# Kernel tuning notes

Hardware: AMD Instinct MI355X
Metric: run time of the kernel (lower is better)

Reference implementation:

```python
import jax, jax.numpy as jnp
import numpy as np

D_MODEL = 1024
D_INNER = 2048   # expand * d_model
D_STATE = 16
D_CONV = 4
DT_RANK = 64     # ceil(d_model / 16)
BATCH = 2
SEQLEN = 4096


def setup_inputs() -> dict:
    key = jax.random.key(0)
    ks = jax.random.split(key, 9)
    g = lambda k, shape, scale: jax.random.normal(k, shape, dtype=jnp.float32) * scale
    hidden_states = g(ks[0], (BATCH, SEQLEN, D_MODEL), 1.0)
    W_in = g(ks[1], (2 * D_INNER, D_MODEL), D_MODEL ** -0.5)
    conv_w = g(ks[2], (D_INNER, D_CONV), D_CONV ** -0.5)
    conv_b = g(ks[3], (D_INNER,), 0.02)
    x_proj_w = g(ks[4], (DT_RANK + 2 * D_STATE, D_INNER), D_INNER ** -0.5)
    dt_w = g(ks[5], (D_INNER, DT_RANK), DT_RANK ** -0.5)
    # dt bias init as in Mamba: inverse softplus of dt ~ U[log(1e-3), log(1e-1)]
    dt = jnp.exp(jax.random.uniform(ks[6], (D_INNER,), dtype=jnp.float32)
                 * (np.log(0.1) - np.log(0.001)) + np.log(0.001))
    dt = jnp.clip(dt, 1e-4, None)
    dt_b = dt + jnp.log(-jnp.expm1(-dt))
    # A_log init: log of [1..d_state] repeated per channel
    A_log = jnp.log(jnp.tile(jnp.arange(1, D_STATE + 1, dtype=jnp.float32), (D_INNER, 1)))
    D = jnp.ones((D_INNER,), dtype=jnp.float32)
    W_out = g(ks[7], (D_MODEL, D_INNER), D_INNER ** -0.5)
    return dict(hidden_states=hidden_states, W_in=W_in, conv_w=conv_w, conv_b=conv_b,
                x_proj_w=x_proj_w, dt_w=dt_w, dt_b=dt_b, A_log=A_log, D=D, W_out=W_out)


def reference(hidden_states, W_in, conv_w, conv_b, x_proj_w, dt_w, dt_b, A_log, D, W_out):
    B, L, _ = hidden_states.shape
    # in_proj + transpose -> (B, 2*Din, L)
    xz = jnp.einsum('bld,ed->bel', hidden_states, W_in)
    # nanotron (tp=1) splits via view(B, d_inner, 2, L): interleaved channels
    xz = xz.reshape(B, D_INNER, 2, L)
    x, z = xz[:, :, 0, :], xz[:, :, 1, :]          # (B, Din, L)
    # causal depthwise conv1d (pad left d_conv-1) + SiLU
    xc = jax.lax.conv_general_dilated(
        x, conv_w[:, None, :], window_strides=(1,), padding=[(D_CONV - 1, 0)],
        dimension_numbers=('NCH', 'OIH', 'NCH'), feature_group_count=D_INNER)
    x = jax.nn.silu(xc + conv_b[None, :, None])     # (B, Din, L)
    # x_proj -> dt, B, C
    x_dbl = jnp.einsum('bdl,ed->ble', x, x_proj_w)  # (B, L, dt_rank+2N)
    dt, Bm, Cm = jnp.split(x_dbl, [DT_RANK, DT_RANK + D_STATE], axis=-1)
    delta = jnp.einsum('blr,dr->bdl', dt, dt_w)     # (B, Din, L)
    delta = jax.nn.softplus(delta + dt_b[None, :, None])
    A = -jnp.exp(A_log)                             # (Din, N)
    # selective scan over time
    xs = (jnp.transpose(delta, (2, 0, 1)),          # (L, B, Din)
          jnp.transpose(x, (2, 0, 1)),              # (L, B, Din)
          jnp.transpose(Bm, (1, 0, 2)),             # (L, B, N)
          jnp.transpose(Cm, (1, 0, 2)))             # (L, B, N)

    def step(s, inp):
        d_t, x_t, B_t, C_t = inp
        s = s * jnp.exp(d_t[:, :, None] * A[None]) + (d_t * x_t)[:, :, None] * B_t[:, None, :]
        y_t = jnp.einsum('bdn,bn->bd', s, C_t)
        return s, y_t

    s0 = jnp.zeros((B, D_INNER, D_STATE), dtype=hidden_states.dtype)
    _, ys = jax.lax.scan(step, s0, xs)              # ys: (L, B, Din)
    y = jnp.transpose(ys, (1, 2, 0))                # (B, Din, L)
    y = y + D[None, :, None] * x
    y = y * jax.nn.silu(z)
    out = jnp.einsum('bdl,md->blm', y, W_out)       # (B, L, d_model)
    return out
```

## Files before the change

kernel.cpp:

```cpp
#include <hip/hip_runtime.h>
#include <hip/hip_bf16.h>

#define D_MODEL 1024
#define D_INNER 2048
#define D_STATE 16
#define DT_RANK 64
#define BATCH 2
#define SEQLEN 4096
#define BL (BATCH * SEQLEN)
#define NPROJ (DT_RANK + 2 * D_STATE)
#define CH 64
#define NCH (SEQLEN / CH)

typedef __attribute__((ext_vector_type(8))) short bf16x8;
typedef __attribute__((ext_vector_type(4))) float f32x4;
struct S4 { short x, y, z, w; };

__device__ __forceinline__ float sigmoidf_(float v) {
    return 1.0f / (1.0f + __expf(-v));
}

__device__ __forceinline__ unsigned short bf16_rne(float f) {
    unsigned u = __float_as_uint(f);
    unsigned r = u + 0x7FFFu + ((u >> 16) & 1u);
    return (unsigned short)(r >> 16);
}

__device__ __forceinline__ float bf2f(short s) {
    return __uint_as_float(((unsigned)(unsigned short)s) << 16);
}

__global__ __launch_bounds__(256)
void cvt_split(const float* __restrict__ in, short* __restrict__ hi,
               short* __restrict__ lo, int n4) {
    const int i = blockIdx.x * 256 + threadIdx.x;
    if (i >= n4) return;
    const float4 v = reinterpret_cast<const float4*>(in)[i];
    const float f[4] = {v.x, v.y, v.z, v.w};
    S4 h, l;
    short hb[4], lb[4];
#pragma unroll
    for (int j = 0; j < 4; ++j) {
        const unsigned short hh = bf16_rne(f[j]);
        const float hf = __uint_as_float((unsigned)hh << 16);
        hb[j] = (short)hh;
        lb[j] = (short)bf16_rne(f[j] - hf);
    }
    h.x = hb[0]; h.y = hb[1]; h.z = hb[2]; h.w = hb[3];
    l.x = lb[0]; l.y = lb[1]; l.z = lb[2]; l.w = lb[3];
    *reinterpret_cast<S4*>(hi + (size_t)i * 4) = h;
    *reinterpret_cast<S4*>(lo + (size_t)i * 4) = l;
}

__global__ __launch_bounds__(256)
void gemm_bf16x3(const short* __restrict__ Ahi, const short* __restrict__ Alo,
                 const short* __restrict__ Bhi, const short* __restrict__ Blo,
                 float* __restrict__ C, int K, int lda, int ldb, int ldc) {
    __shared__ short sA[2][128][32];
    __shared__ short sB[2][128][32];
    const int t = threadIdx.x;
    const int w = t >> 6, l = t & 63;

    const int nwg = gridDim.x * gridDim.y;
    int bid = blockIdx.y * gridDim.x + blockIdx.x;
    if ((nwg & 7) == 0) bid = (bid & 7) * (nwg >> 3) + (bid >> 3);
    const int m0 = (bid / gridDim.x) * 128, n0 = (bid % gridDim.x) * 128;
    const int wr = w >> 1, wc = w & 1;

    const short* gsrc;
    short* sdst;
    int ld, tile0;
    if (w == 0)      { gsrc = Ahi; sdst = &sA[0][0][0]; tile0 = m0; ld = lda; }
    else if (w == 1) { gsrc = Alo; sdst = &sA[1][0][0]; tile0 = m0; ld = lda; }
    else if (w == 2) { gsrc = Bhi; sdst = &sB[0][0][0]; tile0 = n0; ld = ldb; }
    else             { gsrc = Blo; sdst = &sB[1][0][0]; tile0 = n0; ld = ldb; }
    const size_t grow = (size_t)(tile0 + (l >> 2)) * ld + ((l & 3) << 3);

    f32x4 acc[4][4] = {};
    const int frow = l & 15;
    const int kb = (l >> 4) << 3;

    for (int k0 = 0; k0 < K; k0 += 32) {
        __syncthreads();
#pragma unroll
        for (int i = 0; i < 8; ++i) {
            const short* g = gsrc + grow + (size_t)(i << 4) * ld + k0;
            __builtin_amdgcn_global_load_lds(
                (const __attribute__((address_space(1))) void*)g,
                (__attribute__((address_space(3))) void*)(sdst + (i << 9)),
                16, 0, 0);
        }
        __syncthreads();

        bf16x8 a[2][4], b[2][4];
#pragma unroll
        for (int f = 0; f < 4; ++f) {
            a[0][f] = *reinterpret_cast<const bf16x8*>(&sA[0][wr * 64 + f * 16 + frow][kb]);
            a[1][f] = *reinterpret_cast<const bf16x8*>(&sA[1][wr * 64 + f * 16 + frow][kb]);
            b[0][f] = *reinterpret_cast<const bf16x8*>(&sB[0][wc * 64 + f * 16 + frow][kb]);
            b[1][f] = *reinterpret_cast<const bf16x8*>(&sB[1][wc * 64 + f * 16 + frow][kb]);
        }
#pragma unroll
        for (int fi = 0; fi < 4; ++fi)
#pragma unroll
            for (int fj = 0; fj < 4; ++fj) {
                acc[fi][fj] = __builtin_amdgcn_mfma_f32_16x16x32_bf16(
                    a[0][fi], b[0][fj], acc[fi][fj], 0, 0, 0);
                acc[fi][fj] = __builtin_amdgcn_mfma_f32_16x16x32_bf16(
                    a[1][fi], b[0][fj], acc[fi][fj], 0, 0, 0);
                acc[fi][fj] = __builtin_amdgcn_mfma_f32_16x16x32_bf16(
                    a[0][fi], b[1][fj], acc[fi][fj], 0, 0, 0);
            }
    }

    const int crow = (l >> 4) << 2;
    const int ccol = l & 15;
#pragma unroll
    for (int fi = 0; fi < 4; ++fi)
#pragma unroll
        for (int fj = 0; fj < 4; ++fj)
#pragma unroll
            for (int r = 0; r < 4; ++r)
                C[(size_t)(m0 + wr * 64 + fi * 16 + crow + r) * ldc
                  + (n0 + wc * 64 + fj * 16 + ccol)] = acc[fi][fj][r];
}

__global__ __launch_bounds__(256)
void gemm96(const short* __restrict__ Xhi, const short* __restrict__ Xlo,
            const short* __restrict__ Whi, const short* __restrict__ Wlo,
            float* __restrict__ C) {
    const int t = threadIdx.x;
    const int w = t >> 6, l = t & 63;
    const int m0 = blockIdx.x * 32;
    const int rfrag = (w >> 1) * 16;
    const int cbase = (w & 1) * 48;
    const int lrow = l & 15;
    const int koff0 = (l >> 4) << 3;
    f32x4 acc[3] = {};
    const size_t arow = (size_t)(m0 + rfrag + lrow) * D_INNER;
#pragma unroll 2
    for (int k0 = 0; k0 < D_INNER; k0 += 32) {
        const int ko = k0 + koff0;
        const bf16x8 ah = *reinterpret_cast<const bf16x8*>(Xhi + arow + ko);
        const bf16x8 al = *reinterpret_cast<const bf16x8*>(Xlo + arow + ko);
#pragma unroll
        for (int jj = 0; jj < 3; ++jj) {
            const size_t brow = (size_t)(cbase + jj * 16 + lrow) * D_INNER + ko;
            const bf16x8 bh = *reinterpret_cast<const bf16x8*>(Whi + brow);
            const bf16x8 bl = *reinterpret_cast<const bf16x8*>(Wlo + brow);
            acc[jj] = __builtin_amdgcn_mfma_f32_16x16x32_bf16(ah, bh, acc[jj], 0, 0, 0);
            acc[jj] = __builtin_amdgcn_mfma_f32_16x16x32_bf16(al, bh, acc[jj], 0, 0, 0);
            acc[jj] = __builtin_amdgcn_mfma_f32_16x16x32_bf16(ah, bl, acc[jj], 0, 0, 0);
        }
    }
    const int crow = (l >> 4) << 2;
#pragma unroll
    for (int jj = 0; jj < 3; ++jj)
#pragma unroll
        for (int r = 0; r < 4; ++r)
            C[(size_t)(m0 + rfrag + crow + r) * NPROJ + cbase + jj * 16 + lrow] = acc[jj][r];
}

template <int EPI>
__global__ __launch_bounds__(256)
void gemm_nt(const float* __restrict__ A, const float* __restrict__ B,
             float* __restrict__ C, int M, int N, int K,
             int lda, int ldb, int ldc, const float* __restrict__ bias) {
    constexpr int BM = 64, BN = 64, BK = 16, PAD = 4;
    __shared__ float As[BK][BM + PAD];
    __shared__ float Bs[BK][BN + PAD];
    const int t = threadIdx.x;
    const int tx = t & 15, ty = t >> 4;
    const int m0 = blockIdx.y * BM, n0 = blockIdx.x * BN;
    const int lrow = t >> 2;
    const int lcol = (t & 3) * 4;

    float acc[4][4] = {{0.f}};

    for (int k0 = 0; k0 < K; k0 += BK) {
        float4 av = *reinterpret_cast<const float4*>(
            A + (size_t)(m0 + lrow) * lda + k0 + lcol);
        float4 bv = *reinterpret_cast<const float4*>(
            B + (size_t)(n0 + lrow) * ldb + k0 + lcol);
        __syncthreads();
        As[lcol + 0][lrow] = av.x; As[lcol + 1][lrow] = av.y;
        As[lcol + 2][lrow] = av.z; As[lcol + 3][lrow] = av.w;
        Bs[lcol + 0][lrow] = bv.x; Bs[lcol + 1][lrow] = bv.y;
        Bs[lcol + 2][lrow] = bv.z; Bs[lcol + 3][lrow] = bv.w;
        __syncthreads();
#pragma unroll
        for (int k = 0; k < BK; ++k) {
            float4 a = *reinterpret_cast<const float4*>(&As[k][ty * 4]);
            float4 b = *reinterpret_cast<const float4*>(&Bs[k][tx * 4]);
            float ar[4] = {a.x, a.y, a.z, a.w};
            float br[4] = {b.x, b.y, b.z, b.w};
#pragma unroll
            for (int i = 0; i < 4; ++i)
#pragma unroll
                for (int j = 0; j < 4; ++j)
                    acc[i][j] = fmaf(ar[i], br[j], acc[i][j]);
        }
    }

#pragma unroll
    for (int i = 0; i < 4; ++i) {
        const int m = m0 + ty * 4 + i;
#pragma unroll
        for (int j = 0; j < 4; ++j) {
            const int n = n0 + tx * 4 + j;
            float v = acc[i][j];
            if (EPI == 1) {
                v += bias[n];
                v = fmaxf(v, 0.f) + log1pf(__expf(-fabsf(v)));
            }
            C[(size_t)m * ldc + n] = v;
        }
    }
}

__global__ __launch_bounds__(256)
void conv_silu_k(const float* __restrict__ xr, const float* __restrict__ cw,
                 const float* __restrict__ cb, short* __restrict__ xchi,
                 short* __restrict__ xclo) {
    const int idx = blockIdx.x * 256 + threadIdx.x;
    const int d = idx & (D_INNER - 1);
    const int bl = idx >> 11;
    const int l = bl & (SEQLEN - 1);
    const float4 w4 = *reinterpret_cast<const float4*>(cw + (size_t)d * 4);
    const float wj[4] = {w4.x, w4.y, w4.z, w4.w};
    float acc = cb[d];
#pragma unroll
    for (int j = 0; j < 4; ++j) {
        const int ll = l - 3 + j;
        if (ll >= 0)
            acc += xr[(size_t)(bl - 3 + j) * D_INNER + d] * wj[j];
    }
    const float v = acc * sigmoidf_(acc);
    const unsigned short hh = bf16_rne(v);
    xchi[idx] = (short)hh;
    xclo[idx] = (short)bf16_rne(v - __uint_as_float((unsigned)hh << 16));
}

__global__ __launch_bounds__(256)
void scan1(const float* __restrict__ delta, const short* __restrict__ xchi,
           const short* __restrict__ xclo, const float* __restrict__ dtbc,
           const float* __restrict__ A_log, float* __restrict__ sum_delta,
           float* __restrict__ S_end) {
    const int d = blockIdx.x * 256 + threadIdx.x;
    const int b = blockIdx.y;
    const int c = blockIdx.z;
    __shared__ float bc[CH][32];
    for (int i = threadIdx.x; i < CH * 32; i += 256) {
        const int row = i >> 5, col = i & 31;
        bc[row][col] = dtbc[(size_t)(b * SEQLEN + c * CH + row) * NPROJ + DT_RANK + col];
    }
    __syncthreads();
    float A[16];
#pragma unroll
    for (int n = 0; n < 16; ++n) A[n] = -__expf(A_log[(size_t)d * 16 + n]);
    float s[16] = {0.f};
    float sd = 0.f;
    const size_t base = ((size_t)b * SEQLEN + (size_t)c * CH) * D_INNER + d;
    for (int li = 0; li < CH; ++li) {
        const size_t o = base + (size_t)li * D_INNER;
        const float dl = delta[o];
        const float xv = bf2f(xchi[o]) + bf2f(xclo[o]);
        sd += dl;
        const float dx = dl * xv;
#pragma unroll
        for (int n = 0; n < 16; ++n) {
            const float a = __expf(dl * A[n]);
            s[n] = fmaf(s[n], a, dx * bc[li][n]);
        }
    }
    sum_delta[((size_t)c * BATCH + b) * D_INNER + d] = sd;
#pragma unroll
    for (int n = 0; n < 16; ++n)
        S_end[(((size_t)c * BATCH + b) * 16 + n) * D_INNER + d] = s[n];
}

__global__ __launch_bounds__(256)
void scan2(const float* __restrict__ sum_delta, float* __restrict__ S,
           const float* __restrict__ A_log) {
    const int idx = blockIdx.x * 256 + threadIdx.x;
    const int d = idx & (D_INNER - 1);
    const int n = (idx >> 11) & 15;
    const int b = idx >> 15;
    const float A = -__expf(A_log[(size_t)d * 16 + n]);
    float carry = 0.f;
    for (int c = 0; c < NCH; ++c) {
        const float sd = sum_delta[((size_t)c * BATCH + b) * D_INNER + d];
        const size_t o = (((size_t)c * BATCH + b) * 16 + n) * D_INNER + d;
        const float se = S[o];
        S[o] = carry;
        carry = fmaf(carry, __expf(sd * A), se);
    }
}

__global__ __launch_bounds__(256)
void scan3(float* __restrict__ delta ,
           const short* __restrict__ xchi, const short* __restrict__ xclo,
           const float* __restrict__ z, const float* __restrict__ dtbc,
           const float* __restrict__ A_log, const float* __restrict__ S_init,
           const float* __restrict__ Dp) {
    const int d = blockIdx.x * 256 + threadIdx.x;
    const int b = blockIdx.y;
    const int c = blockIdx.z;
    __shared__ float bc[CH][32];
    for (int i = threadIdx.x; i < CH * 32; i += 256) {
        const int row = i >> 5, col = i & 31;
        bc[row][col] = dtbc[(size_t)(b * SEQLEN + c * CH + row) * NPROJ + DT_RANK + col];
    }
    __syncthreads();
    float A[16];
#pragma unroll
    for (int n = 0; n < 16; ++n) A[n] = -__expf(A_log[(size_t)d * 16 + n]);
    float s[16];
#pragma unroll
    for (int n = 0; n < 16; ++n)
        s[n] = S_init[(((size_t)c * BATCH + b) * 16 + n) * D_INNER + d];
    const float Dv = Dp[d];
    const size_t base = ((size_t)b * SEQLEN + (size_t)c * CH) * D_INNER + d;
    for (int li = 0; li < CH; ++li) {
        const size_t o = base + (size_t)li * D_INNER;
        const float dl = delta[o];
        const float xv = bf2f(xchi[o]) + bf2f(xclo[o]);
        const float dx = dl * xv;
        float y = 0.f;
#pragma unroll
        for (int n = 0; n < 16; ++n) {
            const float a = __expf(dl * A[n]);
            s[n] = fmaf(s[n], a, dx * bc[li][n]);
            y = fmaf(s[n], bc[li][16 + n], y);
        }
        const float zv = z[o];
        delta[o] = (y + Dv * xv) * (zv * sigmoidf_(zv));
    }
}

extern "C" void kernel_launch(void* const* d_in, const int* in_sizes, int n_in,
                              void* d_out, int out_size, void* d_ws, size_t ws_size,
                              hipStream_t stream) {
    const float* hidden   = (const float*)d_in[0];
    const float* W_in     = (const float*)d_in[1];
    const float* conv_w   = (const float*)d_in[2];
    const float* conv_b   = (const float*)d_in[3];
    const float* x_proj_w = (const float*)d_in[4];
    const float* dt_w     = (const float*)d_in[5];
    const float* dt_b     = (const float*)d_in[6];
    const float* A_log    = (const float*)d_in[7];
    const float* Dp       = (const float*)d_in[8];
    const float* W_out    = (const float*)d_in[9];
    float* out = (float*)d_out;

    float* ws    = (float*)d_ws;
    float* xbuf  = ws;
    float* zbuf  = xbuf + (size_t)BL * D_INNER;
    float* xcreg = zbuf + (size_t)BL * D_INNER;
    float* dtbc  = xcreg + (size_t)BL * D_INNER;
    float* sumd  = dtbc + (size_t)BL * NPROJ;
    float* Send  = sumd + (size_t)NCH * BATCH * D_INNER;
    float* xpw   = Send + (size_t)NCH * BATCH * 16 * D_INNER;

    short* hxhi  = (short*)xcreg;
    short* hxlo  = hxhi + (size_t)BL * D_MODEL;
    short* winhi = hxlo + (size_t)BL * D_MODEL;
    short* winlo = winhi + (size_t)2 * D_INNER * D_MODEL;
    short* xpwhi = (short*)xpw;
    short* xpwlo = xpwhi + (size_t)NPROJ * D_INNER;

    const dim3 thr(256);

    cvt_split<<<dim3(BL * D_MODEL / 1024), thr, 0, stream>>>(hidden, hxhi, hxlo, BL * D_MODEL / 4);
    cvt_split<<<dim3(2 * D_INNER * D_MODEL / 1024), thr, 0, stream>>>(W_in, winhi, winlo, 2 * D_INNER * D_MODEL / 4);
    cvt_split<<<dim3(NPROJ * D_INNER / 1024), thr, 0, stream>>>(x_proj_w, xpwhi, xpwlo, NPROJ * D_INNER / 4);

    gemm_bf16x3<<<dim3(D_INNER / 128, BL / 128), thr, 0, stream>>>(
        hxhi, hxlo, winhi, winlo, xbuf, D_MODEL, D_MODEL, 2 * D_MODEL, D_INNER);
    gemm_bf16x3<<<dim3(D_INNER / 128, BL / 128), thr, 0, stream>>>(
        hxhi, hxlo, winhi + D_MODEL, winlo + D_MODEL, zbuf, D_MODEL, D_MODEL, 2 * D_MODEL, D_INNER);

    short* xchi = (short*)xcreg;
    short* xclo = xchi + (size_t)BL * D_INNER;
    conv_silu_k<<<dim3(BL * D_INNER / 256), thr, 0, stream>>>(xbuf, conv_w, conv_b, xchi, xclo);

    gemm96<<<dim3(BL / 32), thr, 0, stream>>>(xchi, xclo, xpwhi, xpwlo, dtbc);

    gemm_nt<1><<<dim3(D_INNER / 64, BL / 64), thr, 0, stream>>>(
        dtbc, dt_w, xbuf, BL, D_INNER, DT_RANK, NPROJ, DT_RANK, D_INNER, dt_b);

    scan1<<<dim3(D_INNER / 256, BATCH, NCH), thr, 0, stream>>>(
        xbuf, xchi, xclo, dtbc, A_log, sumd, Send);
    scan2<<<dim3(BATCH * 16 * D_INNER / 256), thr, 0, stream>>>(sumd, Send, A_log);
    scan3<<<dim3(D_INNER / 256, BATCH, NCH), thr, 0, stream>>>(
        xbuf, xchi, xclo, zbuf, dtbc, A_log, Send, Dp);

    short* yhi  = (short*)zbuf;
    short* ylo  = yhi + (size_t)BL * D_INNER;
    short* wohi = (short*)xcreg;
    short* wolo = wohi + (size_t)D_MODEL * D_INNER;
    cvt_split<<<dim3(BL * D_INNER / 1024), thr, 0, stream>>>(xbuf, yhi, ylo, BL * D_INNER / 4);
    cvt_split<<<dim3(D_MODEL * D_INNER / 1024), thr, 0, stream>>>(W_out, wohi, wolo, D_MODEL * D_INNER / 4);

    gemm_bf16x3<<<dim3(D_MODEL / 128, BL / 128), thr, 0, stream>>>(
        yhi, ylo, wohi, wolo, out, D_INNER, D_INNER, D_INNER, D_MODEL);
}
```

Baseline: 790.2 us.

## Swizzle GEMM LDS, move delta GEMM to MFMA, fuse y bf16 split into scan

Adds an XOR swizzle to the global-to-LDS load layout and the fragment reads of the bf16x3 GEMM to cut LDS bank conflicts. The fp32 SIMT delta GEMM (K=64) is replaced by the split-bf16 MFMA GEMM with a fused bias+softplus epilogue, and gemm96 now writes the dt columns as hi/lo bf16 directly. scan3 writes y already split into hi/lo bf16 into the xc buffers, which removes the separate cvt_split pass over y before the output projection. The trade-off is extra workspace for the dt and dt_w splits and reuse of buffers that must stay in the right order.

Result: faster. 762.9 us (-3.5%).

```diff
diff --git a/kernel.cpp b/kernel.cpp
--- a/kernel.cpp
+++ b/kernel.cpp
@@ -52,10 +52,12 @@
     *reinterpret_cast<S4*>(lo + (size_t)i * 4) = l;
 }
 
+template <int EPI>
 __global__ __launch_bounds__(256)
 void gemm_bf16x3(const short* __restrict__ Ahi, const short* __restrict__ Alo,
                  const short* __restrict__ Bhi, const short* __restrict__ Blo,
-                 float* __restrict__ C, int K, int lda, int ldb, int ldc) {
+                 float* __restrict__ C, int K, int lda, int ldb, int ldc,
+                 const float* __restrict__ bias) {
     __shared__ short sA[2][128][32];
     __shared__ short sB[2][128][32];
     const int t = threadIdx.x;
@@ -74,11 +76,12 @@
     else if (w == 1) { gsrc = Alo; sdst = &sA[1][0][0]; tile0 = m0; ld = lda; }
     else if (w == 2) { gsrc = Bhi; sdst = &sB[0][0][0]; tile0 = n0; ld = ldb; }
     else             { gsrc = Blo; sdst = &sB[1][0][0]; tile0 = n0; ld = ldb; }
-    const size_t grow = (size_t)(tile0 + (l >> 2)) * ld + ((l & 3) << 3);
+    const int kc_src = ((l & 3) ^ ((l >> 3) & 3)) << 3;
+    const size_t grow = (size_t)(tile0 + (l >> 2)) * ld + kc_src;
 
     f32x4 acc[4][4] = {};
     const int frow = l & 15;
-    const int kb = (l >> 4) << 3;
+    const int kb = (((l >> 4) ^ ((frow >> 1) & 3)) << 3);
 
     for (int k0 = 0; k0 < K; k0 += 32) {
         __syncthreads();
@@ -118,17 +121,25 @@
 #pragma unroll
     for (int fi = 0; fi < 4; ++fi)
 #pragma unroll
-        for (int fj = 0; fj < 4; ++fj)
-#pragma unroll
-            for (int r = 0; r < 4; ++r)
-                C[(size_t)(m0 + wr * 64 + fi * 16 + crow + r) * ldc
-                  + (n0 + wc * 64 + fj * 16 + ccol)] = acc[fi][fj][r];
+        for (int fj = 0; fj < 4; ++fj) {
+            const int n = n0 + wc * 64 + fj * 16 + ccol;
+#pragma unroll
+            for (int r = 0; r < 4; ++r) {
+                float v = acc[fi][fj][r];
+                if (EPI == 1) {
+                    v += bias[n];
+                    v = fmaxf(v, 0.f) + log1pf(__expf(-fabsf(v)));
+                }
+                C[(size_t)(m0 + wr * 64 + fi * 16 + crow + r) * ldc + n] = v;
+            }
+        }
 }
 
 __global__ __launch_bounds__(256)
 void gemm96(const short* __restrict__ Xhi, const short* __restrict__ Xlo,
             const short* __restrict__ Whi, const short* __restrict__ Wlo,
-            float* __restrict__ C) {
+            float* __restrict__ C, short* __restrict__ dthi,
+            short* __restrict__ dtlo) {
     const int t = threadIdx.x;
     const int w = t >> 6, l = t & 63;
     const int m0 = blockIdx.x * 32;
@@ -155,65 +166,19 @@
     }
     const int crow = (l >> 4) << 2;
 #pragma unroll
-    for (int jj = 0; jj < 3; ++jj)
-#pragma unroll
-        for (int r = 0; r < 4; ++r)
-            C[(size_t)(m0 + rfrag + crow + r) * NPROJ + cbase + jj * 16 + lrow] = acc[jj][r];
-}
-
-template <int EPI>
-__global__ __launch_bounds__(256)
-void gemm_nt(const float* __restrict__ A, const float* __restrict__ B,
-             float* __restrict__ C, int M, int N, int K,
-             int lda, int ldb, int ldc, const float* __restrict__ bias) {
-    constexpr int BM = 64, BN = 64, BK = 16, PAD = 4;
-    __shared__ float As[BK][BM + PAD];
-    __shared__ float Bs[BK][BN + PAD];
-    const int t = threadIdx.x;
-    const int tx = t & 15, ty = t >> 4;
-    const int m0 = blockIdx.y * BM, n0 = blockIdx.x * BN;
-    const int lrow = t >> 2;
-    const int lcol = (t & 3) * 4;
-
-    float acc[4][4] = {{0.f}};
-
-    for (int k0 = 0; k0 < K; k0 += BK) {
-        float4 av = *reinterpret_cast<const float4*>(
-            A + (size_t)(m0 + lrow) * lda + k0 + lcol);
-        float4 bv = *reinterpret_cast<const float4*>(
-            B + (size_t)(n0 + lrow) * ldb + k0 + lcol);
-        __syncthreads();
-        As[lcol + 0][lrow] = av.x; As[lcol + 1][lrow] = av.y;
-        As[lcol + 2][lrow] = av.z; As[lcol + 3][lrow] = av.w;
-        Bs[lcol + 0][lrow] = bv.x; Bs[lcol + 1][lrow] = bv.y;
-        Bs[lcol + 2][lrow] = bv.z; Bs[lcol + 3][lrow] = bv.w;
-        __syncthreads();
-#pragma unroll
-        for (int k = 0; k < BK; ++k) {
-            float4 a = *reinterpret_cast<const float4*>(&As[k][ty * 4]);
-            float4 b = *reinterpret_cast<const float4*>(&Bs[k][tx * 4]);
-            float ar[4] = {a.x, a.y, a.z, a.w};
-            float br[4] = {b.x, b.y, b.z, b.w};
-#pragma unroll
-            for (int i = 0; i < 4; ++i)
-#pragma unroll
-                for (int j = 0; j < 4; ++j)
-                    acc[i][j] = fmaf(ar[i], br[j], acc[i][j]);
-        }
-    }
-
-#pragma unroll
-    for (int i = 0; i < 4; ++i) {
-        const int m = m0 + ty * 4 + i;
-#pragma unroll
-        for (int j = 0; j < 4; ++j) {
-            const int n = n0 + tx * 4 + j;
-            float v = acc[i][j];
-            if (EPI == 1) {
-                v += bias[n];
-                v = fmaxf(v, 0.f) + log1pf(__expf(-fabsf(v)));
+    for (int jj = 0; jj < 3; ++jj) {
+        const int col = cbase + jj * 16 + lrow;
+#pragma unroll
+        for (int r = 0; r < 4; ++r) {
+            const int m = m0 + rfrag + crow + r;
+            const float v = acc[jj][r];
+            C[(size_t)m * NPROJ + col] = v;
+            if (col < DT_RANK) {
+                const unsigned short hh = bf16_rne(v);
+                dthi[(size_t)m * DT_RANK + col] = (short)hh;
+                dtlo[(size_t)m * DT_RANK + col] =
+                    (short)bf16_rne(v - __uint_as_float((unsigned)hh << 16));
             }
-            C[(size_t)m * ldc + n] = v;
         }
     }
 }
@@ -298,11 +263,10 @@
 }
 
 __global__ __launch_bounds__(256)
-void scan3(float* __restrict__ delta ,
-           const short* __restrict__ xchi, const short* __restrict__ xclo,
-           const float* __restrict__ z, const float* __restrict__ dtbc,
-           const float* __restrict__ A_log, const float* __restrict__ S_init,
-           const float* __restrict__ Dp) {
+void scan3(const float* __restrict__ delta, short* __restrict__ xchi,
+           short* __restrict__ xclo, const float* __restrict__ z,
+           const float* __restrict__ dtbc, const float* __restrict__ A_log,
+           const float* __restrict__ S_init, const float* __restrict__ Dp) {
     const int d = blockIdx.x * 256 + threadIdx.x;
     const int b = blockIdx.y;
     const int c = blockIdx.z;
@@ -334,7 +298,10 @@
             y = fmaf(s[n], bc[li][16 + n], y);
         }
         const float zv = z[o];
-        delta[o] = (y + Dv * xv) * (zv * sigmoidf_(zv));
+        const float yv = (y + Dv * xv) * (zv * sigmoidf_(zv));
+        const unsigned short hh = bf16_rne(yv);
+        xchi[o] = (short)hh;
+        xclo[o] = (short)bf16_rne(yv - __uint_as_float((unsigned)hh << 16));
     }
 }
 
@@ -360,34 +327,39 @@
     float* dtbc  = xcreg + (size_t)BL * D_INNER;
     float* sumd  = dtbc + (size_t)BL * NPROJ;
     float* Send  = sumd + (size_t)NCH * BATCH * D_INNER;
-    float* xpw   = Send + (size_t)NCH * BATCH * 16 * D_INNER;
+
+    short* xpwhi = (short*)(Send + (size_t)NCH * BATCH * 16 * D_INNER);
+    short* xpwlo = xpwhi + (size_t)NPROJ * D_INNER;
+    short* dtwhi = xpwlo + (size_t)NPROJ * D_INNER;
+    short* dtwlo = dtwhi + (size_t)D_INNER * DT_RANK;
+    short* dthi  = dtwlo + (size_t)D_INNER * DT_RANK;
+    short* dtlo  = dthi + (size_t)BL * DT_RANK;
 
     short* hxhi  = (short*)xcreg;
     short* hxlo  = hxhi + (size_t)BL * D_MODEL;
     short* winhi = hxlo + (size_t)BL * D_MODEL;
     short* winlo = winhi + (size_t)2 * D_INNER * D_MODEL;
-    short* xpwhi = (short*)xpw;
-    short* xpwlo = xpwhi + (size_t)NPROJ * D_INNER;
 
     const dim3 thr(256);
 
     cvt_split<<<dim3(BL * D_MODEL / 1024), thr, 0, stream>>>(hidden, hxhi, hxlo, BL * D_MODEL / 4);
     cvt_split<<<dim3(2 * D_INNER * D_MODEL / 1024), thr, 0, stream>>>(W_in, winhi, winlo, 2 * D_INNER * D_MODEL / 4);
     cvt_split<<<dim3(NPROJ * D_INNER / 1024), thr, 0, stream>>>(x_proj_w, xpwhi, xpwlo, NPROJ * D_INNER / 4);
-
-    gemm_bf16x3<<<dim3(D_INNER / 128, BL / 128), thr, 0, stream>>>(
-        hxhi, hxlo, winhi, winlo, xbuf, D_MODEL, D_MODEL, 2 * D_MODEL, D_INNER);
-    gemm_bf16x3<<<dim3(D_INNER / 128, BL / 128), thr, 0, stream>>>(
-        hxhi, hxlo, winhi + D_MODEL, winlo + D_MODEL, zbuf, D_MODEL, D_MODEL, 2 * D_MODEL, D_INNER);
+    cvt_split<<<dim3(D_INNER * DT_RANK / 1024), thr, 0, stream>>>(dt_w, dtwhi, dtwlo, D_INNER * DT_RANK / 4);
+
+    gemm_bf16x3<0><<<dim3(D_INNER / 128, BL / 128), thr, 0, stream>>>(
+        hxhi, hxlo, winhi, winlo, xbuf, D_MODEL, D_MODEL, 2 * D_MODEL, D_INNER, nullptr);
+    gemm_bf16x3<0><<<dim3(D_INNER / 128, BL / 128), thr, 0, stream>>>(
+        hxhi, hxlo, winhi + D_MODEL, winlo + D_MODEL, zbuf, D_MODEL, D_MODEL, 2 * D_MODEL, D_INNER, nullptr);
 
     short* xchi = (short*)xcreg;
     short* xclo = xchi + (size_t)BL * D_INNER;
     conv_silu_k<<<dim3(BL * D_INNER / 256), thr, 0, stream>>>(xbuf, conv_w, conv_b, xchi, xclo);
 
-    gemm96<<<dim3(BL / 32), thr, 0, stream>>>(xchi, xclo, xpwhi, xpwlo, dtbc);
-
-    gemm_nt<1><<<dim3(D_INNER / 64, BL / 64), thr, 0, stream>>>(
-        dtbc, dt_w, xbuf, BL, D_INNER, DT_RANK, NPROJ, DT_RANK, D_INNER, dt_b);
+    gemm96<<<dim3(BL / 32), thr, 0, stream>>>(xchi, xclo, xpwhi, xpwlo, dtbc, dthi, dtlo);
+
+    gemm_bf16x3<1><<<dim3(D_INNER / 128, BL / 128), thr, 0, stream>>>(
+        dthi, dtlo, dtwhi, dtwlo, xbuf, DT_RANK, DT_RANK, DT_RANK, D_INNER, dt_b);
 
     scan1<<<dim3(D_INNER / 256, BATCH, NCH), thr, 0, stream>>>(
         xbuf, xchi, xclo, dtbc, A_log, sumd, Send);
@@ -395,13 +367,10 @@
     scan3<<<dim3(D_INNER / 256, BATCH, NCH), thr, 0, stream>>>(
         xbuf, xchi, xclo, zbuf, dtbc, A_log, Send, Dp);
 
-    short* yhi  = (short*)zbuf;
-    short* ylo  = yhi + (size_t)BL * D_INNER;
-    short* wohi = (short*)xcreg;
+    short* wohi = (short*)zbuf;
     short* wolo = wohi + (size_t)D_MODEL * D_INNER;
-    cvt_split<<<dim3(BL * D_INNER / 1024), thr, 0, stream>>>(xbuf, yhi, ylo, BL * D_INNER / 4);
     cvt_split<<<dim3(D_MODEL * D_INNER / 1024), thr, 0, stream>>>(W_out, wohi, wolo, D_MODEL * D_INNER / 4);
 
-    gemm_bf16x3<<<dim3(D_MODEL / 128, BL / 128), thr, 0, stream>>>(
-        yhi, ylo, wohi, wolo, out, D_INNER, D_INNER, D_INNER, D_MODEL);
-}
+    gemm_bf16x3<0><<<dim3(D_MODEL / 128, BL / 128), thr, 0, stream>>>(
+        xchi, xclo, wohi, wolo, out, D_INNER, D_INNER, D_INNER, D_MODEL, nullptr);
+}
```
